# Kernel optimization log

Hardware: AMD Instinct MI355X
Metric: run time of the kernel (lower is better)

Reference implementation:

```python
import jax, jax.numpy as jnp
import numpy as np
import math

EMBED_DIM = 768
NUM_HEADS = 12
MLP_HIDDEN = int(EMBED_DIM * 2.0)
LN_EPS = 1e-6


def _complex_linear(r, i, wr, wi, br, bi):
    # (r + i*j) @ (wr + wi*j)^T + (br + bi*j)
    out_r = r @ wr.T - i @ wi.T + br
    out_i = r @ wi.T + i @ wr.T + bi
    return out_r, out_i


def _complex_layernorm(r, i, gamma, beta):
    # magnitude-based LN over feature dim; gamma/beta: [F, 2]
    mag = jnp.sqrt(r * r + i * i + LN_EPS)           # [..., F]
    mean = mag.mean(axis=-1, keepdims=True)
    var = ((mag - mean) ** 2).mean(axis=-1, keepdims=True)  # unbiased=False
    norm_mag = (mag - mean) / jnp.sqrt(var + LN_EPS)
    scale = norm_mag / (mag + LN_EPS)
    r_n = r * scale
    i_n = i * scale
    return gamma[..., 0] * r_n + beta[..., 0], gamma[..., 1] * i_n + beta[..., 1]


def setup_inputs() -> dict:
    key = jax.random.key(0)
    ks = jax.random.split(key, 12)
    B, N, E, H = 2, 2048, EMBED_DIM, MLP_HIDDEN
    std_qkv = math.sqrt(2.0 / (E + 3 * E))
    std_proj = math.sqrt(2.0 / (E + E))
    std_fc1 = math.sqrt(2.0 / (E + H))
    std_fc2 = math.sqrt(2.0 / (H + E))
    inp = {
        "x": jax.random.normal(ks[0], (B, N, 2 * E), dtype=jnp.float32),
        "norm1_gamma": 1.0 + 0.1 * jax.random.normal(ks[1], (E, 2), dtype=jnp.float32),
        "norm1_beta": 0.1 * jax.random.normal(ks[2], (E, 2), dtype=jnp.float32),
        "qkv_wr": std_qkv * jax.random.normal(ks[3], (3 * E, E), dtype=jnp.float32),
        "qkv_wi": std_qkv * jax.random.normal(ks[4], (3 * E, E), dtype=jnp.float32),
        "qkv_br": jnp.zeros((3 * E,), dtype=jnp.float32),
        "qkv_bi": jnp.zeros((3 * E,), dtype=jnp.float32),
        "proj_wr": std_proj * jax.random.normal(ks[5], (E, E), dtype=jnp.float32),
        "proj_wi": std_proj * jax.random.normal(ks[6], (E, E), dtype=jnp.float32),
        "proj_br": jnp.zeros((E,), dtype=jnp.float32),
        "proj_bi": jnp.zeros((E,), dtype=jnp.float32),
        "norm2_gamma": 1.0 + 0.1 * jax.random.normal(ks[7], (E, 2), dtype=jnp.float32),
        "norm2_beta": 0.1 * jax.random.normal(ks[8], (E, 2), dtype=jnp.float32),
        "fc1_wr": std_fc1 * jax.random.normal(ks[9], (H, E), dtype=jnp.float32),
        "fc1_wi": std_fc1 * jax.random.normal(ks[10], (H, E), dtype=jnp.float32),
        "fc1_br": jnp.zeros((H,), dtype=jnp.float32),
        "fc1_bi": jnp.zeros((H,), dtype=jnp.float32),
        "fc2_wr": std_fc2 * jax.random.normal(ks[11], (E, H), dtype=jnp.float32),
        "fc2_wi": std_fc2 * jax.random.normal(jax.random.fold_in(key, 99), (E, H), dtype=jnp.float32),
        "fc2_br": jnp.zeros((E,), dtype=jnp.float32),
        "fc2_bi": jnp.zeros((E,), dtype=jnp.float32),
    }
    return inp


def reference(x, norm1_gamma, norm1_beta, qkv_wr, qkv_wi, qkv_br, qkv_bi,
              proj_wr, proj_wi, proj_br, proj_bi, norm2_gamma, norm2_beta,
              fc1_wr, fc1_wi, fc1_br, fc1_bi, fc2_wr, fc2_wi, fc2_br, fc2_bi):
    B, N, _ = x.shape
    E, nH = EMBED_DIM, NUM_HEADS
    hd = E // nH
    xc = x.reshape(B, N, E, 2)
    xr, xi = xc[..., 0], xc[..., 1]

    # --- attention branch ---
    nr, ni = _complex_layernorm(xr, xi, norm1_gamma, norm1_beta)
    qkv_r, qkv_i = _complex_linear(nr, ni, qkv_wr, qkv_wi, qkv_br, qkv_bi)  # [B,N,3E]
    # split to [3, B, nH, N, hd]
    def split_heads(t):
        return t.reshape(B, N, 3, nH, hd).transpose(2, 0, 3, 1, 4)
    qkv_r = split_heads(qkv_r)
    qkv_i = split_heads(qkv_i)
    qr, kr, vr = qkv_r[0], qkv_r[1], qkv_r[2]
    qi, ki, vi = qkv_i[0], qkv_i[1], qkv_i[2]

    # complex attention scores: q * conj-free formulation per source
    attn_real = jnp.einsum('bhqd,bhkd->bhqk', qr, kr) + jnp.einsum('bhqd,bhkd->bhqk', qi, ki)
    attn_imag = jnp.einsum('bhqd,bhkd->bhqk', qr, ki) - jnp.einsum('bhqd,bhkd->bhqk', qi, kr)
    attn_mag = jnp.sqrt(attn_real ** 2 + attn_imag ** 2 + 1e-8) / math.sqrt(hd)
    attn_w = jax.nn.softmax(attn_mag, axis=-1)
    out_r = jnp.einsum('bhqk,bhkd->bhqd', attn_w, vr)
    out_i = jnp.einsum('bhqk,bhkd->bhqd', attn_w, vi)
    # [B,nH,N,hd] -> [B,N,E]
    out_r = out_r.transpose(0, 2, 1, 3).reshape(B, N, E)
    out_i = out_i.transpose(0, 2, 1, 3).reshape(B, N, E)
    pr, pi = _complex_linear(out_r, out_i, proj_wr, proj_wi, proj_br, proj_bi)
    xr = xr + pr
    xi = xi + pi

    # --- MLP branch ---
    nr2, ni2 = _complex_layernorm(xr, xi, norm2_gamma, norm2_beta)
    h_r, h_i = _complex_linear(nr2, ni2, fc1_wr, fc1_wi, fc1_br, fc1_bi)
    h_r = jax.nn.gelu(h_r, approximate=False)
    h_i = jax.nn.gelu(h_i, approximate=False)
    m_r, m_i = _complex_linear(h_r, h_i, fc2_wr, fc2_wi, fc2_br, fc2_bi)
    xr = xr + m_r
    xi = xi + m_i

    return jnp.stack([xr, xi], axis=-1).reshape(B, N, 2 * E)
```

## Files before the change

### kernel.cpp

```cpp
#include <hip/hip_runtime.h>
#include <cmath>

typedef __bf16 bf16;
typedef __bf16 bf16x8 __attribute__((ext_vector_type(8)));
typedef __bf16 bf16x4 __attribute__((ext_vector_type(4)));
typedef float  f32x4  __attribute__((ext_vector_type(4)));
typedef unsigned int u32x4 __attribute__((ext_vector_type(4)));

#define MFMA16(a, b, c) __builtin_amdgcn_mfma_f32_16x16x32_bf16((a), (b), (c), 0, 0, 0)
#define LOG2E 1.44269504088896f

static __device__ __forceinline__ void gl_lds16(const void* g, void* l) {
    __builtin_amdgcn_global_load_lds((const __attribute__((address_space(1))) void*)g,
                                     (__attribute__((address_space(3))) void*)l, 16, 0, 0);
}

static __device__ __forceinline__ bf16x8 bneg8(bf16x8 x) {
    u32x4 u = __builtin_bit_cast(u32x4, x);
    u = u ^ 0x80008000u;
    return __builtin_bit_cast(bf16x8, u);
}

static __device__ __forceinline__ f32x4 zero4() {
    return f32x4{0.0f, 0.0f, 0.0f, 0.0f};
}

__global__ void fill_kernel(float* p, float v, int n) {
    for (int i = blockIdx.x * blockDim.x + threadIdx.x; i < n; i += gridDim.x * blockDim.x)
        p[i] = v;
}

struct Cvt8 {
    const float* s[8];
    bf16* d[8];
    int boff[9];
};
__global__ __launch_bounds__(256) void cvt8_kernel(Cvt8 c) {
    int blk = blockIdx.x;
    int seg = 0;
#pragma unroll
    for (int k = 0; k < 7; ++k)
        if (blk >= c.boff[k + 1]) seg = k + 1;
    const int local = blk - c.boff[seg];
    const int i = local * 1024 + threadIdx.x * 4;
    const float4 v = *(const float4*)(c.s[seg] + i);
    bf16x4 o;
    o[0] = (bf16)v.x; o[1] = (bf16)v.y; o[2] = (bf16)v.z; o[3] = (bf16)v.w;
    *(bf16x4*)(c.d[seg] + i) = o;
}

template <int SRC>
__global__ __launch_bounds__(256) void cln_kernel(
    const void* __restrict__ xa, const void* __restrict__ xb,
    const float* __restrict__ gamma, const float* __restrict__ beta,
    bf16* __restrict__ nr, bf16* __restrict__ ni) {
    __shared__ float red[4];
    const int t = threadIdx.x;
    const size_t base = (size_t)blockIdx.x * 768;

    float r[3], im[3], mg[3];
#pragma unroll
    for (int j = 0; j < 3; ++j) {
        const int f = t + j * 256;
        if (SRC == 1) {
            const float2 v = ((const float2*)xa)[base + f];
            r[j] = v.x;
            im[j] = v.y;
        } else {
            r[j] = (float)((const bf16*)xa)[base + f];
            im[j] = (float)((const bf16*)xb)[base + f];
        }
        mg[j] = __builtin_amdgcn_sqrtf(r[j] * r[j] + im[j] * im[j] + 1e-6f);
    }
    float s = mg[0] + mg[1] + mg[2];
#pragma unroll
    for (int m = 32; m >= 1; m >>= 1) s += __shfl_xor(s, m);
    if ((t & 63) == 0) red[t >> 6] = s;
    __syncthreads();
    const float mean = (red[0] + red[1] + red[2] + red[3]) * (1.0f / 768.0f);
    __syncthreads();

    float v2 = 0.0f;
#pragma unroll
    for (int j = 0; j < 3; ++j) {
        const float d = mg[j] - mean;
        v2 += d * d;
    }
#pragma unroll
    for (int m = 32; m >= 1; m >>= 1) v2 += __shfl_xor(v2, m);
    if ((t & 63) == 0) red[t >> 6] = v2;
    __syncthreads();
    const float var = (red[0] + red[1] + red[2] + red[3]) * (1.0f / 768.0f);
    const float rstd = rsqrtf(var + 1e-6f);

#pragma unroll
    for (int j = 0; j < 3; ++j) {
        const int f = t + j * 256;
        const float sc = (mg[j] - mean) * rstd / (mg[j] + 1e-6f);
        nr[base + f] = (bf16)(gamma[2 * f] * (r[j] * sc) + beta[2 * f]);
        ni[base + f] = (bf16)(gamma[2 * f + 1] * (im[j] * sc) + beta[2 * f + 1]);
    }
}

template <int BM, int BN, int MODE, int OCC, bool SWZC>
__global__ __launch_bounds__(256, OCC) void cgemm_kernel(
    const bf16* __restrict__ Ar, const bf16* __restrict__ Ai,
    const bf16* __restrict__ Wr, const bf16* __restrict__ Wi,
    const float* __restrict__ br, const float* __restrict__ bi,
    const void* __restrict__ resr, const void* __restrict__ resi,
    float* __restrict__ outFr, float* __restrict__ outFi,
    bf16* __restrict__ outBr, bf16* __restrict__ outBi,
    int N, int K) {
    constexpr int MR = BM / 32;
    constexpr int NR = BN / 32;
    constexpr int ASEG = BM / 8;
    constexpr int NSEG = (BM + BN) / 8;
    constexpr int SPW = NSEG / 4;

    __shared__ __align__(16) bf16 sA[2][BM][64];
    __shared__ __align__(16) bf16 sB[2][BN][64];

    const int tid = threadIdx.x;
    const int wave = tid >> 6, lane = tid & 63;
    const int lg = lane >> 4, lr = lane & 15;

    const int bid = blockIdx.y * gridDim.x + blockIdx.x;
    const int xcd = bid & 7;
    const int i = bid >> 3;
    int rowb, colb;
    if (SWZC) {
        const int cpx = gridDim.y >> 3;
        colb = xcd * cpx + (i % cpx);
        rowb = i / cpx;
    } else {
        const int rpx = gridDim.x >> 3;
        rowb = xcd * rpx + (i % rpx);
        colb = i / rpx;
    }
    const int row0 = rowb * BM, col0 = colb * BN;

    const int wm = (wave >> 1) * (BM / 2), wn = (wave & 1) * (BN / 2);

    const int srow = lane >> 3;
    const int schunk = (lane & 7) ^ srow;
    const int spl = schunk >> 2;
    const int sc8 = (schunk & 3) * 8;

    auto issue = [&](int buf, int kt) {
#pragma unroll
        for (int s = 0; s < SPW; ++s) {
            const int id = wave * SPW + s;
            if (id < ASEG) {
                const int row = id * 8 + srow;
                gl_lds16((spl ? Ai : Ar) + (size_t)(row0 + row) * K + kt + sc8,
                         &sA[buf][id * 8][0]);
            } else {
                const int row = (id - ASEG) * 8 + srow;
                gl_lds16((spl ? Wi : Wr) + (size_t)(col0 + row) * K + kt + sc8,
                         &sB[buf][(id - ASEG) * 8][0]);
            }
        }
    };

    f32x4 accr[MR][NR], acci[MR][NR];
#pragma unroll
    for (int a = 0; a < MR; ++a)
#pragma unroll
        for (int b2 = 0; b2 < NR; ++b2) {
            accr[a][b2] = zero4();
            acci[a][b2] = zero4();
        }

    issue(0, 0);

    const int KT = K / 32;
    for (int kt = 0; kt < KT; ++kt) {
        const int buf = kt & 1;
        if (kt + 1 < KT) {
            issue(buf ^ 1, (kt + 1) * 32);
            __builtin_amdgcn_sched_barrier(0);
            if constexpr (SPW == 8)
                asm volatile("s_waitcnt vmcnt(8)" ::: "memory");
            else if constexpr (SPW == 6)
                asm volatile("s_waitcnt vmcnt(6)" ::: "memory");
            else
                asm volatile("s_waitcnt vmcnt(0)" ::: "memory");
        } else {
            asm volatile("s_waitcnt vmcnt(0)" ::: "memory");
        }
        __builtin_amdgcn_sched_barrier(0);
        __builtin_amdgcn_s_barrier();
        __builtin_amdgcn_sched_barrier(0);

        bf16x8 ar[MR], ai[MR], an[MR];
#pragma unroll
        for (int mt = 0; mt < MR; ++mt) {
            const int rr = wm + mt * 16 + lr;
            const int slr = lg ^ (rr & 7);
            const int sli = (4 + lg) ^ (rr & 7);
            ar[mt] = *(const bf16x8*)(&sA[buf][rr][slr * 8]);
            ai[mt] = *(const bf16x8*)(&sA[buf][rr][sli * 8]);
            an[mt] = bneg8(ai[mt]);
        }
        __builtin_amdgcn_s_setprio(1);
#pragma unroll
        for (int nt = 0; nt < NR; ++nt) {
            const int rr = wn + nt * 16 + lr;
            const int slr = lg ^ (rr & 7);
            const int sli = (4 + lg) ^ (rr & 7);
            const bf16x8 br8 = *(const bf16x8*)(&sB[buf][rr][slr * 8]);
            const bf16x8 bi8 = *(const bf16x8*)(&sB[buf][rr][sli * 8]);
#pragma unroll
            for (int mt = 0; mt < MR; ++mt) {
                accr[mt][nt] = MFMA16(ar[mt], br8, accr[mt][nt]);
                accr[mt][nt] = MFMA16(an[mt], bi8, accr[mt][nt]);
                acci[mt][nt] = MFMA16(ar[mt], bi8, acci[mt][nt]);
                acci[mt][nt] = MFMA16(ai[mt], br8, acci[mt][nt]);
            }
        }
        __builtin_amdgcn_s_setprio(0);
    }

#pragma unroll
    for (int nt = 0; nt < NR; ++nt) {
        const int col = col0 + wn + nt * 16 + lr;
        const float bre = (MODE == 4) ? 0.0f : br[col];
        const float bie = (MODE == 4) ? 0.0f : bi[col];
#pragma unroll
        for (int mt = 0; mt < MR; ++mt) {
#pragma unroll
            for (int j = 0; j < 4; ++j) {
                const int row = row0 + wm + mt * 16 + lg * 4 + j;
                float vr = accr[mt][nt][j];
                float vi = acci[mt][nt][j];
                if (MODE == 4) {
                    vr += br[row];
                    vi += bi[row];
                } else {
                    vr += bre;
                    vi += bie;
                }
                const size_t o = (size_t)row * N + col;
                if (MODE == 0 || MODE == 4) {
                    outBr[o] = (bf16)vr;
                    outBi[o] = (bf16)vi;
                } else if (MODE == 1) {
                    const float2 rv = ((const float2*)resr)[(size_t)row * 768 + col];
                    outBr[o] = (bf16)(rv.x + vr);
                    outBi[o] = (bf16)(rv.y + vi);
                } else if (MODE == 2) {
                    const float t2r = fmaf(vr * vr, 0.044715f, 1.0f);
                    const float er = __builtin_amdgcn_exp2f(vr * t2r * 2.3022082f);
                    vr = vr - vr * __builtin_amdgcn_rcpf(er + 1.0f);
                    const float t2i = fmaf(vi * vi, 0.044715f, 1.0f);
                    const float ei = __builtin_amdgcn_exp2f(vi * t2i * 2.3022082f);
                    vi = vi - vi * __builtin_amdgcn_rcpf(ei + 1.0f);
                    outBr[o] = (bf16)vr;
                    outBi[o] = (bf16)vi;
                } else {
                    const size_t ro = (size_t)row * 768 + col;
                    outFr[(size_t)row * 1536 + 2 * col] =
                        (float)((const bf16*)resr)[ro] + vr;
                    outFr[(size_t)row * 1536 + 2 * col + 1] =
                        (float)((const bf16*)resi)[ro] + vi;
                }
            }
        }
    }
}

__global__ __launch_bounds__(256, 3) void cattn_kernel(
    const bf16* __restrict__ qkr, const bf16* __restrict__ qki,
    const bf16* __restrict__ vtr, const bf16* __restrict__ vti,
    bf16* __restrict__ aor, bf16* __restrict__ aoi) {
    __shared__ __align__(16) bf16 sK[2][2][32][64];
    __shared__ __align__(16) bf16 sV[3][64][64];
    __shared__ __align__(16) bf16 sP[4][16][40];

    const int tid = threadIdx.x;
    const int w = tid >> 6, lane = tid & 63;
    const int lg = lane >> 4, lr = lane & 15;

    const int bid = blockIdx.x;
    const int xcd = bid & 7;
    const int i = bid >> 3;
    const int grp = xcd * 3 + (i >> 5);
    const int qb = i & 31;
    const int h = grp % 12, b = grp / 12;
    const int ld = 1536;

    const int s_krow = lane >> 3;
    const int s_kch8 = ((lane & 7) ^ s_krow) * 8;
    const int s_vlog = (lane & 7) ^ s_krow;
    const int s_vpl = s_vlog >> 2;
    const int s_vk8 = (s_vlog & 3) * 8;

    const bf16* kbase0 = qkr + (size_t)b * 2048 * ld + 768 + h * 64;
    const bf16* kbase1 = qki + (size_t)b * 2048 * ld + 768 + h * 64;
    const bf16* vbase = (s_vpl ? vti : vtr) + (size_t)(h * 64) * 4096 + b * 2048;

    const bf16* kp0 = kbase0 + (size_t)(w * 8 + s_krow) * ld + s_kch8;
    const bf16* kp1 = kbase1 + (size_t)(w * 8 + s_krow) * ld + s_kch8;
    const bf16* vp0 = vbase + (size_t)(w * 8 + s_krow) * 4096 + s_vk8;
    const bf16* vp1 = vbase + (size_t)((4 + w) * 8 + s_krow) * 4096 + s_vk8;

    auto stage = [&](int kb, int vs) {
        gl_lds16(kp0, &sK[kb][0][w * 8][0]);
        gl_lds16(kp1, &sK[kb][1][w * 8][0]);
        gl_lds16(vp0, &sV[vs][w * 8][0]);
        gl_lds16(vp1, &sV[vs][(4 + w) * 8][0]);
        kp0 += 32 * ld;
        kp1 += 32 * ld;
        vp0 += 32;
        vp1 += 32;
    };

    stage(0, 0);

    const size_t qoff = (size_t)(b * 2048 + qb * 64 + w * 16 + lr) * ld + h * 64;
    bf16x8 aqr[2], aqi[2], aqin[2];
#pragma unroll
    for (int ks = 0; ks < 2; ++ks) {
        aqr[ks] = *(const bf16x8*)(qkr + qoff + ks * 32 + lg * 8);
        aqi[ks] = *(const bf16x8*)(qki + qoff + ks * 32 + lg * 8);
        aqin[ks] = bneg8(aqi[ks]);
    }

    f32x4 our[4], oui[4];
#pragma unroll
    for (int d = 0; d < 4; ++d) {
        our[d] = zero4();
        oui[d] = zero4();
    }
    const float C1 = 0.125f * LOG2E;
    float mrun = -1e30f;
    float lrun_p = 0.0f;
    float thr2 = -1.0f;
    float mC2 = 0.0f;

    bf16x8 pfPrev = __builtin_bit_cast(bf16x8, u32x4{0u, 0u, 0u, 0u});
    int vcur = 0, vlast = 0;
    const int slr = lg ^ (lr & 7);
    const int sli = (4 + lg) ^ (lr & 7);

    for (int kt = 0; kt < 64; ++kt) {
        const int kcur = kt & 1;
        int vnext = vcur + 1;
        if (vnext == 3) vnext = 0;
        if (kt < 63) {
            stage(kcur ^ 1, vnext);
            __builtin_amdgcn_sched_barrier(0);
            asm volatile("s_waitcnt vmcnt(4)" ::: "memory");
        } else {
            asm volatile("s_waitcnt vmcnt(0)" ::: "memory");
        }
        __builtin_amdgcn_sched_barrier(0);
        __builtin_amdgcn_s_barrier();
        __builtin_amdgcn_sched_barrier(0);

        f32x4 str[2], sti[2];
        str[0] = zero4(); str[1] = zero4();
        sti[0] = zero4(); sti[1] = zero4();
        __builtin_amdgcn_s_setprio(1);
#pragma unroll
        for (int t = 0; t < 2; ++t) {
#pragma unroll
            for (int ks = 0; ks < 2; ++ks) {
                const int ch = ((ks << 2) | lg) ^ (lr & 7);
                const bf16x8 kr8 = *(const bf16x8*)(&sK[kcur][0][t * 16 + lr][ch * 8]);
                const bf16x8 ki8 = *(const bf16x8*)(&sK[kcur][1][t * 16 + lr][ch * 8]);
                str[t] = MFMA16(kr8, aqr[ks], str[t]);
                str[t] = MFMA16(ki8, aqi[ks], str[t]);
                sti[t] = MFMA16(ki8, aqr[ks], sti[t]);
                sti[t] = MFMA16(kr8, aqin[ks], sti[t]);
            }
        }
        if (kt > 0) {
#pragma unroll
            for (int d = 0; d < 4; ++d) {
                const bf16x8 vr8 = *(const bf16x8*)(&sV[vlast][d * 16 + lr][slr * 8]);
                const bf16x8 vi8 = *(const bf16x8*)(&sV[vlast][d * 16 + lr][sli * 8]);
                our[d] = MFMA16(pfPrev, vr8, our[d]);
                oui[d] = MFMA16(pfPrev, vi8, oui[d]);
            }
        }
        __builtin_amdgcn_s_setprio(0);

        float v[8];
        float vmax = 0.0f;
#pragma unroll
        for (int t = 0; t < 2; ++t)
#pragma unroll
            for (int j = 0; j < 4; ++j) {
                const float sr = str[t][j], si = sti[t][j];
                const float vv = fmaf(sr, sr, fmaf(si, si, 1e-8f));
                v[t * 4 + j] = vv;
                vmax = fmaxf(vmax, vv);
            }

        if (!__all(vmax <= thr2)) {
            vmax = fmaxf(vmax, __shfl_xor(vmax, 16));
            vmax = fmaxf(vmax, __shfl_xor(vmax, 32));
            const float tm = __builtin_amdgcn_sqrtf(vmax) * 0.125f;
            const float mnew = fmaxf(mrun, tm);
            const float corr = __builtin_amdgcn_exp2f((mrun - mnew) * LOG2E);
            float cj[4];
#pragma unroll
            for (int j = 0; j < 4; ++j) cj[j] = __shfl(corr, lg * 4 + j);
#pragma unroll
            for (int d = 0; d < 4; ++d)
#pragma unroll
                for (int j = 0; j < 4; ++j) {
                    our[d][j] *= cj[j];
                    oui[d][j] *= cj[j];
                }
            lrun_p *= corr;
            mrun = mnew;
            const float m8 = mrun + 8.0f;
            thr2 = 64.0f * m8 * m8;
            mC2 = -mrun * LOG2E;
        }

        float p[8];
        float ls = 0.0f;
#pragma unroll
        for (int i2 = 0; i2 < 8; ++i2) {
            p[i2] = __builtin_amdgcn_exp2f(
                fmaf(__builtin_amdgcn_sqrtf(v[i2]), C1, mC2));
            ls += p[i2];
        }
        lrun_p += ls;

#pragma unroll
        for (int t = 0; t < 2; ++t) {
            bf16x4 pk;
#pragma unroll
            for (int j = 0; j < 4; ++j) pk[j] = (bf16)p[t * 4 + j];
            *(bf16x4*)(&sP[w][lr][t * 16 + lg * 4]) = pk;
        }
        pfPrev = *(const bf16x8*)(&sP[w][lr][lg * 8]);

        vlast = vcur;
        vcur = vnext;
    }

#pragma unroll
    for (int d = 0; d < 4; ++d) {
        const bf16x8 vr8 = *(const bf16x8*)(&sV[vlast][d * 16 + lr][slr * 8]);
        const bf16x8 vi8 = *(const bf16x8*)(&sV[vlast][d * 16 + lr][sli * 8]);
        our[d] = MFMA16(pfPrev, vr8, our[d]);
        oui[d] = MFMA16(pfPrev, vi8, oui[d]);
    }

    float lsum = lrun_p;
    lsum += __shfl_xor(lsum, 16);
    lsum += __shfl_xor(lsum, 32);

    float linv[4];
#pragma unroll
    for (int j = 0; j < 4; ++j) {
        const float lj = __shfl(lsum, lg * 4 + j);
        linv[j] = __builtin_amdgcn_rcpf(lj);
    }
#pragma unroll
    for (int d = 0; d < 4; ++d)
#pragma unroll
        for (int j = 0; j < 4; ++j) {
            const int row = b * 2048 + qb * 64 + w * 16 + lg * 4 + j;
            const int col = h * 64 + d * 16 + lr;
            aor[(size_t)row * 768 + col] = (bf16)(our[d][j] * linv[j]);
            aoi[(size_t)row * 768 + col] = (bf16)(oui[d][j] * linv[j]);
        }
}

extern "C" void kernel_launch(void* const* d_in, const int* in_sizes, int n_in,
                              void* d_out, int out_size, void* d_ws, size_t ws_size,
                              hipStream_t stream) {
    const float* x      = (const float*)d_in[0];
    const float* n1g    = (const float*)d_in[1];
    const float* n1b    = (const float*)d_in[2];
    const float* qkvwr  = (const float*)d_in[3];
    const float* qkvwi  = (const float*)d_in[4];
    const float* qkvbr  = (const float*)d_in[5];
    const float* qkvbi  = (const float*)d_in[6];
    const float* projwr = (const float*)d_in[7];
    const float* projwi = (const float*)d_in[8];
    const float* projbr = (const float*)d_in[9];
    const float* projbi = (const float*)d_in[10];
    const float* n2g    = (const float*)d_in[11];
    const float* n2b    = (const float*)d_in[12];
    const float* fc1wr  = (const float*)d_in[13];
    const float* fc1wi  = (const float*)d_in[14];
    const float* fc1br  = (const float*)d_in[15];
    const float* fc1bi  = (const float*)d_in[16];
    const float* fc2wr  = (const float*)d_in[17];
    const float* fc2wi  = (const float*)d_in[18];
    const float* fc2br  = (const float*)d_in[19];
    const float* fc2bi  = (const float*)d_in[20];

    const int M = 4096, E = 768, E3 = 2304, HH = 1536;

    char* base = (char*)d_ws;
    size_t off = 0;
    auto alloc = [&](size_t bytes) -> void* {
        void* p = base + off;
        off += (bytes + 255) & ~(size_t)255;
        return p;
    };
    bf16* xr2  = (bf16*)alloc((size_t)M * E * 2);
    bf16* xi2  = (bf16*)alloc((size_t)M * E * 2);
    bf16* nr   = (bf16*)alloc((size_t)M * E * 2);
    bf16* ni   = (bf16*)alloc((size_t)M * E * 2);
    bf16* wqr  = (bf16*)alloc((size_t)E3 * E * 2);
    bf16* wqi  = (bf16*)alloc((size_t)E3 * E * 2);
    bf16* wpr  = (bf16*)alloc((size_t)E * E * 2);
    bf16* wpi  = (bf16*)alloc((size_t)E * E * 2);
    bf16* w1r  = (bf16*)alloc((size_t)HH * E * 2);
    bf16* w1i  = (bf16*)alloc((size_t)HH * E * 2);
    bf16* w2r  = (bf16*)alloc((size_t)E * HH * 2);
    bf16* w2i  = (bf16*)alloc((size_t)E * HH * 2);
    bf16* qkr  = (bf16*)alloc((size_t)M * HH * 2);
    bf16* qki  = (bf16*)alloc((size_t)M * HH * 2);
    bf16* vtr  = (bf16*)alloc((size_t)E * M * 2);
    bf16* vti  = (bf16*)alloc((size_t)E * M * 2);
    bf16* aor  = (bf16*)alloc((size_t)M * E * 2);
    bf16* aoi  = (bf16*)alloc((size_t)M * E * 2);
    bf16* hr   = (bf16*)alloc((size_t)M * HH * 2);
    bf16* hi   = (bf16*)alloc((size_t)M * HH * 2);

    if (off > ws_size) {
        fill_kernel<<<1024, 256, 0, stream>>>((float*)d_out, 1.0e9f, out_size);
        return;
    }

    Cvt8 c;
    c.s[0] = qkvwr; c.d[0] = wqr;
    c.s[1] = qkvwi; c.d[1] = wqi;
    c.s[2] = projwr; c.d[2] = wpr;
    c.s[3] = projwi; c.d[3] = wpi;
    c.s[4] = fc1wr; c.d[4] = w1r;
    c.s[5] = fc1wi; c.d[5] = w1i;
    c.s[6] = fc2wr; c.d[6] = w2r;
    c.s[7] = fc2wi; c.d[7] = w2i;
    const int nseg[8] = {E3 * E, E3 * E, E * E, E * E, HH * E, HH * E, E * HH, E * HH};
    int cum = 0;
    for (int k = 0; k < 8; ++k) {
        c.boff[k] = cum;
        cum += nseg[k] / 1024;
    }
    c.boff[8] = cum;
    cvt8_kernel<<<cum, 256, 0, stream>>>(c);

    cln_kernel<1><<<M, 256, 0, stream>>>(x, nullptr, n1g, n1b, nr, ni);
    cgemm_kernel<64, 128, 0, 3, false><<<dim3(64, 12), 256, 0, stream>>>(
        nr, ni, wqr, wqi, qkvbr, qkvbi, nullptr, nullptr, nullptr, nullptr,
        qkr, qki, HH, E);
    cgemm_kernel<64, 128, 4, 3, true><<<dim3(12, 32), 256, 0, stream>>>(
        wqr + (size_t)HH * E, wqi + (size_t)HH * E, nr, ni,
        qkvbr + HH, qkvbi + HH, nullptr, nullptr, nullptr, nullptr,
        vtr, vti, M, E);
    cattn_kernel<<<768, 256, 0, stream>>>(qkr, qki, vtr, vti, aor, aoi);
    cgemm_kernel<128, 64, 1, 3, false><<<dim3(32, 12), 256, 0, stream>>>(
        aor, aoi, wpr, wpi, projbr, projbi, x, nullptr, nullptr, nullptr,
        xr2, xi2, E, E);
    cln_kernel<2><<<M, 256, 0, stream>>>(xr2, xi2, n2g, n2b, nr, ni);
    cgemm_kernel<64, 128, 2, 3, false><<<dim3(64, 12), 256, 0, stream>>>(
        nr, ni, w1r, w1i, fc1br, fc1bi, nullptr, nullptr, nullptr, nullptr,
        hr, hi, HH, E);
    cgemm_kernel<128, 64, 3, 3, false><<<dim3(32, 12), 256, 0, stream>>>(
        hr, hi, w2r, w2i, fc2br, fc2bi, xr2, xi2, (float*)d_out, nullptr,
        nullptr, nullptr, E, HH);
}
```

Baseline: 300.8 us.

## Fuse weight conversion with LN1, merge QK and V-transpose GEMMs, restructure attention pipeline

```diff
diff --git a/kernel.cpp b/kernel.cpp
--- a/kernel.cpp
+++ b/kernel.cpp
@@ -34,24 +34,68 @@
     const float* s[8];
     bf16* d[8];
     int boff[9];
+    int cvtBlocks;
 };
-__global__ __launch_bounds__(256) void cvt8_kernel(Cvt8 c) {
-    int blk = blockIdx.x;
-    int seg = 0;
-#pragma unroll
-    for (int k = 0; k < 7; ++k)
-        if (blk >= c.boff[k + 1]) seg = k + 1;
-    const int local = blk - c.boff[seg];
-    const int i = local * 1024 + threadIdx.x * 4;
-    const float4 v = *(const float4*)(c.s[seg] + i);
-    bf16x4 o;
-    o[0] = (bf16)v.x; o[1] = (bf16)v.y; o[2] = (bf16)v.z; o[3] = (bf16)v.w;
-    *(bf16x4*)(c.d[seg] + i) = o;
-}
-
-template <int SRC>
-__global__ __launch_bounds__(256) void cln_kernel(
-    const void* __restrict__ xa, const void* __restrict__ xb,
+__global__ __launch_bounds__(256) void prep_kernel(
+    Cvt8 c, const float* __restrict__ x,
+    const float* __restrict__ gamma, const float* __restrict__ beta,
+    bf16* __restrict__ nr, bf16* __restrict__ ni) {
+    const int t = threadIdx.x;
+    if ((int)blockIdx.x < c.cvtBlocks) {
+        int blk = blockIdx.x;
+        int seg = 0;
+#pragma unroll
+        for (int k = 0; k < 7; ++k)
+            if (blk >= c.boff[k + 1]) seg = k + 1;
+        const int local = blk - c.boff[seg];
+        const int i = local * 1024 + t * 4;
+        const float4 v = *(const float4*)(c.s[seg] + i);
+        bf16x4 o;
+        o[0] = (bf16)v.x; o[1] = (bf16)v.y; o[2] = (bf16)v.z; o[3] = (bf16)v.w;
+        *(bf16x4*)(c.d[seg] + i) = o;
+        return;
+    }
+    __shared__ float red[4];
+    const size_t base = (size_t)(blockIdx.x - c.cvtBlocks) * 768;
+    float r[3], im[3], mg[3];
+#pragma unroll
+    for (int j = 0; j < 3; ++j) {
+        const int f = t + j * 256;
+        const float2 v = ((const float2*)x)[base + f];
+        r[j] = v.x;
+        im[j] = v.y;
+        mg[j] = __builtin_amdgcn_sqrtf(r[j] * r[j] + im[j] * im[j] + 1e-6f);
+    }
+    float s = mg[0] + mg[1] + mg[2];
+#pragma unroll
+    for (int m = 32; m >= 1; m >>= 1) s += __shfl_xor(s, m);
+    if ((t & 63) == 0) red[t >> 6] = s;
+    __syncthreads();
+    const float mean = (red[0] + red[1] + red[2] + red[3]) * (1.0f / 768.0f);
+    __syncthreads();
+    float v2 = 0.0f;
+#pragma unroll
+    for (int j = 0; j < 3; ++j) {
+        const float d = mg[j] - mean;
+        v2 += d * d;
+    }
+#pragma unroll
+    for (int m = 32; m >= 1; m >>= 1) v2 += __shfl_xor(v2, m);
+    if ((t & 63) == 0) red[t >> 6] = v2;
+    __syncthreads();
+    const float var = (red[0] + red[1] + red[2] + red[3]) * (1.0f / 768.0f);
+    const float rstd = rsqrtf(var + 1e-6f);
+#pragma unroll
+    for (int j = 0; j < 3; ++j) {
+        const int f = t + j * 256;
+        const float sc = (mg[j] - mean) * rstd / (mg[j] + 1e-6f);
+        nr[base + f] = (bf16)(gamma[2 * f] * (r[j] * sc) + beta[2 * f]);
+        ni[base + f] = (bf16)(gamma[2 * f + 1] * (im[j] * sc) + beta[2 * f + 1]);
+    }
+}
+
+__global__ __launch_bounds__(256) void cln2_kernel(
+    const bf16* __restrict__ xa, const bf16* __restrict__ xb,
     const float* __restrict__ gamma, const float* __restrict__ beta,
     bf16* __restrict__ nr, bf16* __restrict__ ni) {
     __shared__ float red[4];
@@ -62,14 +106,8 @@
 #pragma unroll
     for (int j = 0; j < 3; ++j) {
         const int f = t + j * 256;
-        if (SRC == 1) {
-            const float2 v = ((const float2*)xa)[base + f];
-            r[j] = v.x;
-            im[j] = v.y;
-        } else {
-            r[j] = (float)((const bf16*)xa)[base + f];
-            im[j] = (float)((const bf16*)xb)[base + f];
-        }
+        r[j] = (float)xa[base + f];
+        im[j] = (float)xb[base + f];
         mg[j] = __builtin_amdgcn_sqrtf(r[j] * r[j] + im[j] * im[j] + 1e-6f);
     }
     float s = mg[0] + mg[1] + mg[2];
@@ -219,32 +257,27 @@
             }
         }
         __builtin_amdgcn_s_setprio(0);
+
+        if (kt + 1 < KT) {
+            __builtin_amdgcn_sched_barrier(0);
+            __builtin_amdgcn_s_barrier();
+            __builtin_amdgcn_sched_barrier(0);
+        }
     }
 
 #pragma unroll
     for (int nt = 0; nt < NR; ++nt) {
         const int col = col0 + wn + nt * 16 + lr;
-        const float bre = (MODE == 4) ? 0.0f : br[col];
-        const float bie = (MODE == 4) ? 0.0f : bi[col];
+        const float bre = br[col], bie = bi[col];
 #pragma unroll
         for (int mt = 0; mt < MR; ++mt) {
 #pragma unroll
             for (int j = 0; j < 4; ++j) {
                 const int row = row0 + wm + mt * 16 + lg * 4 + j;
-                float vr = accr[mt][nt][j];
-                float vi = acci[mt][nt][j];
-                if (MODE == 4) {
-                    vr += br[row];
-                    vi += bi[row];
-                } else {
-                    vr += bre;
-                    vi += bie;
-                }
+                float vr = accr[mt][nt][j] + bre;
+                float vi = acci[mt][nt][j] + bie;
                 const size_t o = (size_t)row * N + col;
-                if (MODE == 0 || MODE == 4) {
-                    outBr[o] = (bf16)vr;
-                    outBi[o] = (bf16)vi;
-                } else if (MODE == 1) {
+                if (MODE == 1) {
                     const float2 rv = ((const float2*)resr)[(size_t)row * 768 + col];
                     outBr[o] = (bf16)(rv.x + vr);
                     outBi[o] = (bf16)(rv.y + vi);
@@ -269,11 +302,157 @@
     }
 }
 
+__global__ __launch_bounds__(256, 3) void qkvt_kernel(
+    const bf16* __restrict__ nr, const bf16* __restrict__ ni,
+    const bf16* __restrict__ wqr, const bf16* __restrict__ wqi,
+    const float* __restrict__ qbr, const float* __restrict__ qbi,
+    bf16* __restrict__ qkr, bf16* __restrict__ qki,
+    bf16* __restrict__ vtr, bf16* __restrict__ vti) {
+    constexpr int BM = 64, BN = 128, K = 768;
+    constexpr int MR = 2, NR = 4, ASEG = 8, SPW = 6;
+    constexpr int HHE = 1536 * 768;
+
+    __shared__ __align__(16) bf16 sA[2][BM][64];
+    __shared__ __align__(16) bf16 sB[2][BN][64];
+
+    const int tid = threadIdx.x;
+    const int wave = tid >> 6, lane = tid & 63;
+    const int lg = lane >> 4, lr = lane & 15;
+
+    const bool isQK = (int)blockIdx.x < 768;
+    const bf16 *Ar, *Ai, *Wr, *Wi;
+    bf16 *outR, *outI;
+    int N, row0, col0;
+    if (isQK) {
+        const int bid = blockIdx.x;
+        const int xcd = bid & 7, i = bid >> 3;
+        row0 = (xcd * 8 + (i & 7)) * BM;
+        col0 = (i >> 3) * BN;
+        Ar = nr; Ai = ni; Wr = wqr; Wi = wqi;
+        outR = qkr; outI = qki; N = 1536;
+    } else {
+        const int bid = blockIdx.x - 768;
+        const int xcd = bid & 7, i = bid >> 3;
+        col0 = (xcd * 4 + (i & 3)) * BN;
+        row0 = (i >> 2) * BM;
+        Ar = wqr + HHE; Ai = wqi + HHE; Wr = nr; Wi = ni;
+        outR = vtr; outI = vti; N = 4096;
+    }
+
+    const int wm = (wave >> 1) * (BM / 2), wn = (wave & 1) * (BN / 2);
+    const int srow = lane >> 3;
+    const int schunk = (lane & 7) ^ srow;
+    const int spl = schunk >> 2;
+    const int sc8 = (schunk & 3) * 8;
+
+    auto issue = [&](int buf, int kt) {
+#pragma unroll
+        for (int s = 0; s < SPW; ++s) {
+            const int id = wave * SPW + s;
+            if (id < ASEG) {
+                const int row = id * 8 + srow;
+                gl_lds16((spl ? Ai : Ar) + (size_t)(row0 + row) * K + kt + sc8,
+                         &sA[buf][id * 8][0]);
+            } else {
+                const int row = (id - ASEG) * 8 + srow;
+                gl_lds16((spl ? Wi : Wr) + (size_t)(col0 + row) * K + kt + sc8,
+                         &sB[buf][(id - ASEG) * 8][0]);
+            }
+        }
+    };
+
+    f32x4 accr[MR][NR], acci[MR][NR];
+#pragma unroll
+    for (int a = 0; a < MR; ++a)
+#pragma unroll
+        for (int b2 = 0; b2 < NR; ++b2) {
+            accr[a][b2] = zero4();
+            acci[a][b2] = zero4();
+        }
+
+    issue(0, 0);
+
+    const int KT = K / 32;
+    for (int kt = 0; kt < KT; ++kt) {
+        const int buf = kt & 1;
+        if (kt + 1 < KT) {
+            issue(buf ^ 1, (kt + 1) * 32);
+            __builtin_amdgcn_sched_barrier(0);
+            asm volatile("s_waitcnt vmcnt(6)" ::: "memory");
+        } else {
+            asm volatile("s_waitcnt vmcnt(0)" ::: "memory");
+        }
+        __builtin_amdgcn_sched_barrier(0);
+        __builtin_amdgcn_s_barrier();
+        __builtin_amdgcn_sched_barrier(0);
+
+        bf16x8 ar[MR], ai[MR], an[MR];
+#pragma unroll
+        for (int mt = 0; mt < MR; ++mt) {
+            const int rr = wm + mt * 16 + lr;
+            const int slr = lg ^ (rr & 7);
+            const int sli = (4 + lg) ^ (rr & 7);
+            ar[mt] = *(const bf16x8*)(&sA[buf][rr][slr * 8]);
+            ai[mt] = *(const bf16x8*)(&sA[buf][rr][sli * 8]);
+            an[mt] = bneg8(ai[mt]);
+        }
+        __builtin_amdgcn_s_setprio(1);
+#pragma unroll
+        for (int nt = 0; nt < NR; ++nt) {
+            const int rr = wn + nt * 16 + lr;
+            const int slr = lg ^ (rr & 7);
+            const int sli = (4 + lg) ^ (rr & 7);
+            const bf16x8 br8 = *(const bf16x8*)(&sB[buf][rr][slr * 8]);
+            const bf16x8 bi8 = *(const bf16x8*)(&sB[buf][rr][sli * 8]);
+#pragma unroll
+            for (int mt = 0; mt < MR; ++mt) {
+                accr[mt][nt] = MFMA16(ar[mt], br8, accr[mt][nt]);
+                accr[mt][nt] = MFMA16(an[mt], bi8, accr[mt][nt]);
+                acci[mt][nt] = MFMA16(ar[mt], bi8, acci[mt][nt]);
+                acci[mt][nt] = MFMA16(ai[mt], br8, acci[mt][nt]);
+            }
+        }
+        __builtin_amdgcn_s_setprio(0);
+
+        if (kt + 1 < KT) {
+            __builtin_amdgcn_sched_barrier(0);
+            __builtin_amdgcn_s_barrier();
+            __builtin_amdgcn_sched_barrier(0);
+        }
+    }
+
+#pragma unroll
+    for (int nt = 0; nt < NR; ++nt) {
+        const int col = col0 + wn + nt * 16 + lr;
+        const float bre = isQK ? qbr[col] : 0.0f;
+        const float bie = isQK ? qbi[col] : 0.0f;
+#pragma unroll
+        for (int mt = 0; mt < MR; ++mt) {
+#pragma unroll
+            for (int j = 0; j < 4; ++j) {
+                const int row = row0 + wm + mt * 16 + lg * 4 + j;
+                float vr = accr[mt][nt][j];
+                float vi = acci[mt][nt][j];
+                if (isQK) {
+                    vr += bre;
+                    vi += bie;
+                } else {
+                    vr += qbr[1536 + row];
+                    vi += qbi[1536 + row];
+                }
+                const size_t o = (size_t)row * N + col;
+                outR[o] = (bf16)vr;
+                outI[o] = (bf16)vi;
+            }
+        }
+    }
+}
+
 __global__ __launch_bounds__(256, 3) void cattn_kernel(
     const bf16* __restrict__ qkr, const bf16* __restrict__ qki,
     const bf16* __restrict__ vtr, const bf16* __restrict__ vti,
     bf16* __restrict__ aor, bf16* __restrict__ aoi) {
-    __shared__ __align__(16) bf16 sK[2][2][32][64];
+    __shared__ __align__(16) bf16 sK[3][2][32][64];
     __shared__ __align__(16) bf16 sV[3][64][64];
     __shared__ __align__(16) bf16 sP[4][16][40];
 
@@ -304,18 +483,18 @@
     const bf16* vp0 = vbase + (size_t)(w * 8 + s_krow) * 4096 + s_vk8;
     const bf16* vp1 = vbase + (size_t)((4 + w) * 8 + s_krow) * 4096 + s_vk8;
 
-    auto stage = [&](int kb, int vs) {
-        gl_lds16(kp0, &sK[kb][0][w * 8][0]);
-        gl_lds16(kp1, &sK[kb][1][w * 8][0]);
-        gl_lds16(vp0, &sV[vs][w * 8][0]);
-        gl_lds16(vp1, &sV[vs][(4 + w) * 8][0]);
+    auto stage = [&](int slot) {
+        gl_lds16(kp0, &sK[slot][0][w * 8][0]);
+        gl_lds16(kp1, &sK[slot][1][w * 8][0]);
+        gl_lds16(vp0, &sV[slot][w * 8][0]);
+        gl_lds16(vp1, &sV[slot][(4 + w) * 8][0]);
         kp0 += 32 * ld;
         kp1 += 32 * ld;
         vp0 += 32;
         vp1 += 32;
     };
 
-    stage(0, 0);
+    stage(0);
 
     const size_t qoff = (size_t)(b * 2048 + qb * 64 + w * 16 + lr) * ld + h * 64;
     bf16x8 aqr[2], aqi[2], aqin[2];
@@ -338,17 +517,15 @@
     float thr2 = -1.0f;
     float mC2 = 0.0f;
 
-    bf16x8 pfPrev = __builtin_bit_cast(bf16x8, u32x4{0u, 0u, 0u, 0u});
-    int vcur = 0, vlast = 0;
+    int cur = 0;
     const int slr = lg ^ (lr & 7);
     const int sli = (4 + lg) ^ (lr & 7);
 
     for (int kt = 0; kt < 64; ++kt) {
-        const int kcur = kt & 1;
-        int vnext = vcur + 1;
-        if (vnext == 3) vnext = 0;
+        int nxt = cur + 1;
+        if (nxt == 3) nxt = 0;
         if (kt < 63) {
-            stage(kcur ^ 1, vnext);
+            stage(nxt);
             __builtin_amdgcn_sched_barrier(0);
             asm volatile("s_waitcnt vmcnt(4)" ::: "memory");
         } else {
@@ -367,21 +544,12 @@
 #pragma unroll
             for (int ks = 0; ks < 2; ++ks) {
                 const int ch = ((ks << 2) | lg) ^ (lr & 7);
-                const bf16x8 kr8 = *(const bf16x8*)(&sK[kcur][0][t * 16 + lr][ch * 8]);
-                const bf16x8 ki8 = *(const bf16x8*)(&sK[kcur][1][t * 16 + lr][ch * 8]);
+                const bf16x8 kr8 = *(const bf16x8*)(&sK[cur][0][t * 16 + lr][ch * 8]);
+                const bf16x8 ki8 = *(const bf16x8*)(&sK[cur][1][t * 16 + lr][ch * 8]);
                 str[t] = MFMA16(kr8, aqr[ks], str[t]);
                 str[t] = MFMA16(ki8, aqi[ks], str[t]);
                 sti[t] = MFMA16(ki8, aqr[ks], sti[t]);
                 sti[t] = MFMA16(kr8, aqin[ks], sti[t]);
-            }
-        }
-        if (kt > 0) {
-#pragma unroll
-            for (int d = 0; d < 4; ++d) {
-                const bf16x8 vr8 = *(const bf16x8*)(&sV[vlast][d * 16 + lr][slr * 8]);
-                const bf16x8 vi8 = *(const bf16x8*)(&sV[vlast][d * 16 + lr][sli * 8]);
-                our[d] = MFMA16(pfPrev, vr8, our[d]);
-                oui[d] = MFMA16(pfPrev, vi8, oui[d]);
             }
         }
         __builtin_amdgcn_s_setprio(0);
@@ -438,18 +606,19 @@
             for (int j = 0; j < 4; ++j) pk[j] = (bf16)p[t * 4 + j];
             *(bf16x4*)(&sP[w][lr][t * 16 + lg * 4]) = pk;
         }
-        pfPrev = *(const bf16x8*)(&sP[w][lr][lg * 8]);
-
-        vlast = vcur;
-        vcur = vnext;
-    }
-
-#pragma unroll
-    for (int d = 0; d < 4; ++d) {
-        const bf16x8 vr8 = *(const bf16x8*)(&sV[vlast][d * 16 + lr][slr * 8]);
-        const bf16x8 vi8 = *(const bf16x8*)(&sV[vlast][d * 16 + lr][sli * 8]);
-        our[d] = MFMA16(pfPrev, vr8, our[d]);
-        oui[d] = MFMA16(pfPrev, vi8, oui[d]);
+        const bf16x8 pf = *(const bf16x8*)(&sP[w][lr][lg * 8]);
+
+        __builtin_amdgcn_s_setprio(1);
+#pragma unroll
+        for (int d = 0; d < 4; ++d) {
+            const bf16x8 vr8 = *(const bf16x8*)(&sV[cur][d * 16 + lr][slr * 8]);
+            const bf16x8 vi8 = *(const bf16x8*)(&sV[cur][d * 16 + lr][sli * 8]);
+            our[d] = MFMA16(pf, vr8, our[d]);
+            oui[d] = MFMA16(pf, vi8, oui[d]);
+        }
+        __builtin_amdgcn_s_setprio(0);
+
+        cur = nxt;
     }
 
     float lsum = lrun_p;
@@ -549,21 +718,16 @@
         cum += nseg[k] / 1024;
     }
     c.boff[8] = cum;
-    cvt8_kernel<<<cum, 256, 0, stream>>>(c);
-
-    cln_kernel<1><<<M, 256, 0, stream>>>(x, nullptr, n1g, n1b, nr, ni);
-    cgemm_kernel<64, 128, 0, 3, false><<<dim3(64, 12), 256, 0, stream>>>(
-        nr, ni, wqr, wqi, qkvbr, qkvbi, nullptr, nullptr, nullptr, nullptr,
-        qkr, qki, HH, E);
-    cgemm_kernel<64, 128, 4, 3, true><<<dim3(12, 32), 256, 0, stream>>>(
-        wqr + (size_t)HH * E, wqi + (size_t)HH * E, nr, ni,
-        qkvbr + HH, qkvbi + HH, nullptr, nullptr, nullptr, nullptr,
-        vtr, vti, M, E);
+    c.cvtBlocks = cum;
+    prep_kernel<<<cum + M, 256, 0, stream>>>(c, x, n1g, n1b, nr, ni);
+
+    qkvt_kernel<<<1152, 256, 0, stream>>>(nr, ni, wqr, wqi, qkvbr, qkvbi,
+                                          qkr, qki, vtr, vti);
     cattn_kernel<<<768, 256, 0, stream>>>(qkr, qki, vtr, vti, aor, aoi);
     cgemm_kernel<128, 64, 1, 3, false><<<dim3(32, 12), 256, 0, stream>>>(
         aor, aoi, wpr, wpi, projbr, projbi, x, nullptr, nullptr, nullptr,
         xr2, xi2, E, E);
-    cln_kernel<2><<<M, 256, 0, stream>>>(xr2, xi2, n2g, n2b, nr, ni);
+    cln2_kernel<<<M, 256, 0, stream>>>(xr2, xi2, n2g, n2b, nr, ni);
     cgemm_kernel<64, 128, 2, 3, false><<<dim3(64, 12), 256, 0, stream>>>(
         nr, ni, w1r, w1i, fc1br, fc1bi, nullptr, nullptr, nullptr, nullptr,
         hr, hi, HH, E);
```

Result: slower. 335.3 us (+11.5%).
